# Optimization experiments

Hardware: AMD Instinct MI355X
Metric: run time of the kernel (lower is better)

The kernel has to match this reference:

```python
import jax, jax.numpy as jnp
import numpy as np

N, E = 50000, 800000
IN_F, HID, OUT, HEADS = 128, 64, 128, 4
NEG_SLOPE = 0.2


def setup_inputs() -> dict:
    key = jax.random.key(0)
    ks = jax.random.split(key, 10)
    s = 0.05
    return {
        "x": jax.random.normal(ks[0], (N, IN_F), dtype=jnp.float32),
        "edge_index": jax.random.randint(ks[1], (2, E), 0, N, dtype=jnp.int64),
        "W1": jax.random.normal(ks[2], (IN_F, HEADS * HID), dtype=jnp.float32) * s,
        "att_src1": jax.random.normal(ks[3], (HEADS, HID), dtype=jnp.float32) * s,
        "att_dst1": jax.random.normal(ks[4], (HEADS, HID), dtype=jnp.float32) * s,
        "b1": jnp.zeros((HEADS * HID,), dtype=jnp.float32),
        "W2": jax.random.normal(ks[5], (HEADS * HID, OUT), dtype=jnp.float32) * s,
        "att_src2": jax.random.normal(ks[6], (1, OUT), dtype=jnp.float32) * s,
        "att_dst2": jax.random.normal(ks[7], (1, OUT), dtype=jnp.float32) * s,
        "b2": jnp.zeros((OUT,), dtype=jnp.float32),
    }


def _gat_layer(x, W, a_src, a_dst, b, src, dst, heads, out_c):
    n = x.shape[0]
    h = (x @ W).reshape(n, heads, out_c)              # [N, H, C]
    alpha_s = jnp.einsum("nhc,hc->nh", h, a_src)       # [N, H]
    alpha_d = jnp.einsum("nhc,hc->nh", h, a_dst)
    e = jax.nn.leaky_relu(alpha_s[src] + alpha_d[dst], NEG_SLOPE)  # [E, H]
    # scatter-softmax over edges grouped by destination node
    m = jax.ops.segment_max(e, dst, num_segments=n)
    ex = jnp.exp(e - m[dst])
    denom = jax.ops.segment_sum(ex, dst, num_segments=n)
    alpha = ex / denom[dst]                            # [E, H]
    out = jax.ops.segment_sum(alpha[:, :, None] * h[src], dst, num_segments=n)
    return out.reshape(n, heads * out_c) + b


def reference(x, edge_index, W1, att_src1, att_dst1, b1, W2, att_src2, att_dst2, b2):
    n = x.shape[0]
    loop = jnp.arange(n, dtype=edge_index.dtype)       # PyG add_self_loops=True
    src = jnp.concatenate([edge_index[0], loop])
    dst = jnp.concatenate([edge_index[1], loop])
    h = _gat_layer(x, W1, att_src1, att_dst1, b1, src, dst, HEADS, HID)
    h = jax.nn.elu(h)
    out = _gat_layer(h, W2, att_src2, att_dst2, b2, src, dst, 1, OUT)
    return out
```

## Files before the change

kernel.cpp:

```cpp
#include <hip/hip_runtime.h>
#include <hip/hip_bf16.h>

#define NEG_SLOPE 0.2f

typedef short bf16x8 __attribute__((ext_vector_type(8)));
typedef float f32x4 __attribute__((ext_vector_type(4)));
typedef float f32x2 __attribute__((ext_vector_type(2)));

__device__ __forceinline__ float bf2f(unsigned short u) {
    return __uint_as_float(((unsigned int)u) << 16);
}
__device__ __forceinline__ unsigned short f2bf(float f) {
    unsigned int x = __float_as_uint(f);
    unsigned int lsb = (x >> 16) & 1u;
    x += 0x7fffu + lsb;
    return (unsigned short)(x >> 16);
}
__device__ __forceinline__ f32x2 upk(unsigned int u) {
    f32x2 r;
    r.x = __uint_as_float(u << 16);
    r.y = __uint_as_float(u & 0xffff0000u);
    return r;
}

__global__ void cast_w_kernel(const float* __restrict__ W, unsigned short* __restrict__ Wt,
                              int K, int NC) {
    int idx = blockIdx.x * 256 + threadIdx.x;
    if (idx >= K * NC) return;
    int k = idx / NC, n = idx % NC;
    Wt[(size_t)n * K + k] = f2bf(W[idx]);
}


__global__ void degree_kernel(const int* __restrict__ ei, int E, int N,
                              int* __restrict__ deg) {
    int e = blockIdx.x * blockDim.x + threadIdx.x;
    int EA = E + N;
    if (e >= EA) return;
    int dst = (e < E) ? ei[E + e] : (e - E);
    atomicAdd(&deg[dst], 1);
}

__global__ void scan_local(const int* __restrict__ deg, int* __restrict__ offs,
                           int* __restrict__ bsum, int N) {
    __shared__ int wsum[16];
    int tid = threadIdx.x;
    int lane = tid & 63;
    int wave = tid >> 6;
    int i = blockIdx.x * 1024 + tid;
    int v = (i < N) ? deg[i] : 0;
    int x = v;
    #pragma unroll
    for (int off = 1; off < 64; off <<= 1) {
        int t = __shfl_up(x, off);
        if (lane >= off) x += t;
    }
    if (lane == 63) wsum[wave] = x;
    __syncthreads();
    if (wave == 0 && lane < 16) {
        int w = wsum[lane];
        #pragma unroll
        for (int off = 1; off < 16; off <<= 1) {
            int t = __shfl_up(w, off);
            if (lane >= off) w += t;
        }
        wsum[lane] = w;
    }
    __syncthreads();
    int wexcl = (wave > 0) ? wsum[wave - 1] : 0;
    if (i <= N) offs[i] = wexcl + x - v;
    if (tid == 0) bsum[blockIdx.x] = wsum[15];
}

__global__ void scan_bsums(int* __restrict__ bsum, int nb) {
    __shared__ int wsum[16];
    int tid = threadIdx.x;
    int lane = tid & 63;
    int wave = tid >> 6;
    int v = (tid < nb) ? bsum[tid] : 0;
    int x = v;
    #pragma unroll
    for (int off = 1; off < 64; off <<= 1) {
        int t = __shfl_up(x, off);
        if (lane >= off) x += t;
    }
    if (lane == 63) wsum[wave] = x;
    __syncthreads();
    if (wave == 0 && lane < 16) {
        int w = wsum[lane];
        #pragma unroll
        for (int off = 1; off < 16; off <<= 1) {
            int t = __shfl_up(w, off);
            if (lane >= off) w += t;
        }
        wsum[lane] = w;
    }
    __syncthreads();
    int wexcl = (wave > 0) ? wsum[wave - 1] : 0;
    if (tid < nb) bsum[tid] = wexcl + x - v;
}

__global__ void scan_add(int* __restrict__ offs, const int* __restrict__ bsum, int N) {
    int i = blockIdx.x * 1024 + threadIdx.x;
    if (i <= N) offs[i] += bsum[blockIdx.x];
}

__global__ void scatter_kernel(const int* __restrict__ ei, int E, int N,
                               const int* __restrict__ offs, int* __restrict__ cnt,
                               int* __restrict__ col) {
    int e = blockIdx.x * blockDim.x + threadIdx.x;
    int EA = E + N;
    if (e >= EA) return;
    int s, d;
    if (e < E) { s = ei[e]; d = ei[E + e]; }
    else       { s = d = e - E; }
    int pos = offs[d] + atomicAdd(&cnt[d], 1);
    col[pos] = s;
}

__global__ void gemm1_mfma(const float* __restrict__ A,
                           const unsigned short* __restrict__ Wt,
                           const float* __restrict__ att_s, const float* __restrict__ att_d,
                           unsigned short* __restrict__ hb,
                           float* __restrict__ as, float* __restrict__ ad, int M) {
    int wave = threadIdx.x >> 6;
    int lane = threadIdx.x & 63;
    int quad = lane >> 4;
    int l16 = lane & 15;
    int m0 = blockIdx.x * 64 + wave * 16;
    int rowc = min(m0 + l16, M - 1);
    bf16x8 a[4];
    const float* ap = A + (size_t)rowc * 128 + quad * 8;
    #pragma unroll
    for (int kc = 0; kc < 4; ++kc) {
        float4 f0 = *(const float4*)(ap + kc * 32);
        float4 f1 = *(const float4*)(ap + kc * 32 + 4);
        bf16x8 v;
        v[0] = (short)f2bf(f0.x); v[1] = (short)f2bf(f0.y);
        v[2] = (short)f2bf(f0.z); v[3] = (short)f2bf(f0.w);
        v[4] = (short)f2bf(f1.x); v[5] = (short)f2bf(f1.y);
        v[6] = (short)f2bf(f1.z); v[7] = (short)f2bf(f1.w);
        a[kc] = v;
    }
    f32x4 acc[16];
    #pragma unroll
    for (int nt = 0; nt < 16; ++nt) {
        f32x4 c = {0.f, 0.f, 0.f, 0.f};
        const unsigned short* bp = Wt + (size_t)(nt * 16 + l16) * 128 + quad * 8;
        #pragma unroll
        for (int kc = 0; kc < 4; ++kc) {
            bf16x8 b = *(const bf16x8*)(bp + kc * 32);
            c = __builtin_amdgcn_mfma_f32_16x16x32_bf16(a[kc], b, c, 0, 0, 0);
        }
        acc[nt] = c;
    }
    float asv[16], adv[16];
    #pragma unroll
    for (int nt = 0; nt < 16; ++nt) {
        asv[nt] = att_s[nt * 16 + l16];
        adv[nt] = att_d[nt * 16 + l16];
    }
    int srow0 = m0 + quad * 4;
    #pragma unroll
    for (int r = 0; r < 4; ++r) {
        int srow = srow0 + r;
        bool ok = srow < M;
        if (ok) {
            #pragma unroll
            for (int nt = 0; nt < 16; ++nt)
                hb[(size_t)srow * 256 + nt * 16 + l16] = f2bf(acc[nt][r]);
        }
        #pragma unroll
        for (int h = 0; h < 4; ++h) {
            float ps = acc[4 * h][r] * asv[4 * h] + acc[4 * h + 1][r] * asv[4 * h + 1]
                     + acc[4 * h + 2][r] * asv[4 * h + 2] + acc[4 * h + 3][r] * asv[4 * h + 3];
            float pd = acc[4 * h][r] * adv[4 * h] + acc[4 * h + 1][r] * adv[4 * h + 1]
                     + acc[4 * h + 2][r] * adv[4 * h + 2] + acc[4 * h + 3][r] * adv[4 * h + 3];
            #pragma unroll
            for (int off = 1; off < 16; off <<= 1) {
                ps += __shfl_xor(ps, off);
                pd += __shfl_xor(pd, off);
            }
            if (ok && l16 == 0) {
                as[srow * 4 + h] = ps;
                ad[srow * 4 + h] = pd;
            }
        }
    }
}

__global__ void gemm2_mfma(const unsigned short* __restrict__ Ab,
                           const unsigned short* __restrict__ Wt,
                           const float* __restrict__ att_s, const float* __restrict__ att_d,
                           unsigned short* __restrict__ hb,
                           float* __restrict__ as, float* __restrict__ ad, int M) {
    int wave = threadIdx.x >> 6;
    int lane = threadIdx.x & 63;
    int quad = lane >> 4;
    int l16 = lane & 15;
    int m0 = blockIdx.x * 64 + wave * 16;
    int rowc = min(m0 + l16, M - 1);
    bf16x8 a[8];
    const unsigned short* ap = Ab + (size_t)rowc * 256 + quad * 8;
    #pragma unroll
    for (int kc = 0; kc < 8; ++kc) a[kc] = *(const bf16x8*)(ap + kc * 32);
    f32x4 acc[8];
    #pragma unroll
    for (int nt = 0; nt < 8; ++nt) {
        f32x4 c = {0.f, 0.f, 0.f, 0.f};
        const unsigned short* bp = Wt + (size_t)(nt * 16 + l16) * 256 + quad * 8;
        #pragma unroll
        for (int kc = 0; kc < 8; ++kc) {
            bf16x8 b = *(const bf16x8*)(bp + kc * 32);
            c = __builtin_amdgcn_mfma_f32_16x16x32_bf16(a[kc], b, c, 0, 0, 0);
        }
        acc[nt] = c;
    }
    float asv[8], adv[8];
    #pragma unroll
    for (int nt = 0; nt < 8; ++nt) {
        asv[nt] = att_s[nt * 16 + l16];
        adv[nt] = att_d[nt * 16 + l16];
    }
    int srow0 = m0 + quad * 4;
    #pragma unroll
    for (int r = 0; r < 4; ++r) {
        int srow = srow0 + r;
        bool ok = srow < M;
        if (ok) {
            #pragma unroll
            for (int nt = 0; nt < 8; ++nt)
                hb[(size_t)srow * 128 + nt * 16 + l16] = f2bf(acc[nt][r]);
        }
        float ps = 0.f, pd = 0.f;
        #pragma unroll
        for (int nt = 0; nt < 8; ++nt) {
            ps = fmaf(acc[nt][r], asv[nt], ps);
            pd = fmaf(acc[nt][r], adv[nt], pd);
        }
        #pragma unroll
        for (int off = 1; off < 16; off <<= 1) {
            ps += __shfl_xor(ps, off);
            pd += __shfl_xor(pd, off);
        }
        if (ok && l16 == 0) { as[srow] = ps; ad[srow] = pd; }
    }
}

__global__ void agg1_kernel(const unsigned short* __restrict__ hb,
                            const float* __restrict__ as,
                            const float* __restrict__ ad,
                            const int* __restrict__ offs, const int* __restrict__ col,
                            const float* __restrict__ b1,
                            unsigned short* __restrict__ out, int N) {
    int node = blockIdx.x * 4 + (threadIdx.x >> 6);
    if (node >= N) return;
    int lane = threadIdx.x & 63;
    int half = lane >> 5;
    int sub  = lane & 31;
    int head = sub >> 3;
    int c0 = sub * 8;
    float adv = ad[node * 4 + head];
    int beg = offs[node], end = offs[node + 1];
    float d = 0.f;
    f32x2 acc[4] = {};
    int j = beg + half;
    for (; j + 6 < end; j += 8) {
        int s0 = col[j];
        int s1 = col[j + 2];
        int s2 = col[j + 4];
        int s3 = col[j + 6];
        uint4 g0 = *(const uint4*)(hb + (size_t)s0 * 256 + c0);
        uint4 g1 = *(const uint4*)(hb + (size_t)s1 * 256 + c0);
        uint4 g2 = *(const uint4*)(hb + (size_t)s2 * 256 + c0);
        uint4 g3 = *(const uint4*)(hb + (size_t)s3 * 256 + c0);
        float e0 = as[s0 * 4 + head] + adv;
        float e1 = as[s1 * 4 + head] + adv;
        float e2 = as[s2 * 4 + head] + adv;
        float e3 = as[s3 * 4 + head] + adv;
        e0 = (e0 > 0.f) ? e0 : NEG_SLOPE * e0;
        e1 = (e1 > 0.f) ? e1 : NEG_SLOPE * e1;
        e2 = (e2 > 0.f) ? e2 : NEG_SLOPE * e2;
        e3 = (e3 > 0.f) ? e3 : NEG_SLOPE * e3;
        float p0 = __expf(e0), p1 = __expf(e1), p2 = __expf(e2), p3 = __expf(e3);
        d += (p0 + p1) + (p2 + p3);
        const unsigned int* w0 = (const unsigned int*)&g0;
        const unsigned int* w1 = (const unsigned int*)&g1;
        const unsigned int* w2 = (const unsigned int*)&g2;
        const unsigned int* w3 = (const unsigned int*)&g3;
        f32x2 v0 = {p0, p0}, v1 = {p1, p1}, v2 = {p2, p2}, v3 = {p3, p3};
        #pragma unroll
        for (int i = 0; i < 4; ++i) {
            acc[i] = __builtin_elementwise_fma(v0, upk(w0[i]), acc[i]);
            acc[i] = __builtin_elementwise_fma(v1, upk(w1[i]), acc[i]);
            acc[i] = __builtin_elementwise_fma(v2, upk(w2[i]), acc[i]);
            acc[i] = __builtin_elementwise_fma(v3, upk(w3[i]), acc[i]);
        }
    }
    for (; j + 2 < end; j += 4) {
        int s0 = col[j];
        int s1 = col[j + 2];
        uint4 g0 = *(const uint4*)(hb + (size_t)s0 * 256 + c0);
        uint4 g1 = *(const uint4*)(hb + (size_t)s1 * 256 + c0);
        float e0 = as[s0 * 4 + head] + adv;
        float e1 = as[s1 * 4 + head] + adv;
        e0 = (e0 > 0.f) ? e0 : NEG_SLOPE * e0;
        e1 = (e1 > 0.f) ? e1 : NEG_SLOPE * e1;
        float p0 = __expf(e0), p1 = __expf(e1);
        d += p0 + p1;
        const unsigned int* w0 = (const unsigned int*)&g0;
        const unsigned int* w1 = (const unsigned int*)&g1;
        f32x2 v0 = {p0, p0}, v1 = {p1, p1};
        #pragma unroll
        for (int i = 0; i < 4; ++i) {
            acc[i] = __builtin_elementwise_fma(v0, upk(w0[i]), acc[i]);
            acc[i] = __builtin_elementwise_fma(v1, upk(w1[i]), acc[i]);
        }
    }
    for (; j < end; j += 2) {
        int s = col[j];
        uint4 g = *(const uint4*)(hb + (size_t)s * 256 + c0);
        float e = as[s * 4 + head] + adv;
        e = (e > 0.f) ? e : NEG_SLOPE * e;
        float p = __expf(e);
        d += p;
        const unsigned int* w = (const unsigned int*)&g;
        f32x2 v = {p, p};
        #pragma unroll
        for (int i = 0; i < 4; ++i)
            acc[i] = __builtin_elementwise_fma(v, upk(w[i]), acc[i]);
    }
    d += __shfl_xor(d, 32);
    #pragma unroll
    for (int i = 0; i < 4; ++i) {
        acc[i].x += __shfl_xor(acc[i].x, 32);
        acc[i].y += __shfl_xor(acc[i].y, 32);
    }
    if (half == 0) {
        float inv = 1.f / d;
        float4 bb0 = *(const float4*)(b1 + c0);
        float4 bb1 = *(const float4*)(b1 + c0 + 4);
        float av[8] = {acc[0].x, acc[0].y, acc[1].x, acc[1].y,
                       acc[2].x, acc[2].y, acc[3].x, acc[3].y};
        float bb[8] = {bb0.x, bb0.y, bb0.z, bb0.w, bb1.x, bb1.y, bb1.z, bb1.w};
        unsigned short o[8];
        #pragma unroll
        for (int i = 0; i < 8; ++i) {
            float v = av[i] * inv + bb[i];
            v = (v > 0.f) ? v : (__expf(v) - 1.f);
            o[i] = f2bf(v);
        }
        ushort4 p0 = {o[0], o[1], o[2], o[3]};
        ushort4 p1 = {o[4], o[5], o[6], o[7]};
        *(ushort4*)(out + (size_t)node * 256 + c0) = p0;
        *(ushort4*)(out + (size_t)node * 256 + c0 + 4) = p1;
    }
}

__global__ void agg2_kernel(const unsigned short* __restrict__ hb,
                            const float* __restrict__ as,
                            const float* __restrict__ ad,
                            const int* __restrict__ offs, const int* __restrict__ col,
                            const float* __restrict__ b2,
                            float* __restrict__ out, int N) {
    int node = blockIdx.x * 4 + (threadIdx.x >> 6);
    if (node >= N) return;
    int lane = threadIdx.x & 63;
    int q   = lane >> 4;
    int sub = lane & 15;
    int c0 = sub * 8;
    float adv = ad[node];
    int beg = offs[node], end = offs[node + 1];
    float d = 0.f;
    f32x2 acc[4] = {};
    int j = beg + q;
    for (; j + 4 < end; j += 8) {
        int s0 = col[j];
        int s1 = col[j + 4];
        uint4 g0 = *(const uint4*)(hb + (size_t)s0 * 128 + c0);
        uint4 g1 = *(const uint4*)(hb + (size_t)s1 * 128 + c0);
        float e0 = as[s0] + adv;
        float e1 = as[s1] + adv;
        e0 = (e0 > 0.f) ? e0 : NEG_SLOPE * e0;
        e1 = (e1 > 0.f) ? e1 : NEG_SLOPE * e1;
        float p0 = __expf(e0), p1 = __expf(e1);
        d += p0 + p1;
        const unsigned int* w0 = (const unsigned int*)&g0;
        const unsigned int* w1 = (const unsigned int*)&g1;
        f32x2 v0 = {p0, p0}, v1 = {p1, p1};
        #pragma unroll
        for (int i = 0; i < 4; ++i) {
            acc[i] = __builtin_elementwise_fma(v0, upk(w0[i]), acc[i]);
            acc[i] = __builtin_elementwise_fma(v1, upk(w1[i]), acc[i]);
        }
    }
    for (; j < end; j += 4) {
        int s = col[j];
        uint4 g = *(const uint4*)(hb + (size_t)s * 128 + c0);
        float e = as[s] + adv;
        e = (e > 0.f) ? e : NEG_SLOPE * e;
        float p = __expf(e);
        d += p;
        const unsigned int* w = (const unsigned int*)&g;
        f32x2 v = {p, p};
        #pragma unroll
        for (int i = 0; i < 4; ++i)
            acc[i] = __builtin_elementwise_fma(v, upk(w[i]), acc[i]);
    }
    d += __shfl_xor(d, 16);
    d += __shfl_xor(d, 32);
    #pragma unroll
    for (int i = 0; i < 4; ++i) {
        acc[i].x += __shfl_xor(acc[i].x, 16);
        acc[i].x += __shfl_xor(acc[i].x, 32);
        acc[i].y += __shfl_xor(acc[i].y, 16);
        acc[i].y += __shfl_xor(acc[i].y, 32);
    }
    if (lane < 16) {
        float inv = 1.f / d;
        float4 bb0 = *(const float4*)(b2 + c0);
        float4 bb1 = *(const float4*)(b2 + c0 + 4);
        float av[8] = {acc[0].x, acc[0].y, acc[1].x, acc[1].y,
                       acc[2].x, acc[2].y, acc[3].x, acc[3].y};
        float bb[8] = {bb0.x, bb0.y, bb0.z, bb0.w, bb1.x, bb1.y, bb1.z, bb1.w};
        float o[8];
        #pragma unroll
        for (int i = 0; i < 8; ++i) o[i] = av[i] * inv + bb[i];
        *(float4*)(out + (size_t)node * 128 + c0) = make_float4(o[0], o[1], o[2], o[3]);
        *(float4*)(out + (size_t)node * 128 + c0 + 4) = make_float4(o[4], o[5], o[6], o[7]);
    }
}


extern "C" void kernel_launch(void* const* d_in, const int* in_sizes, int n_in,
                              void* d_out, int out_size, void* d_ws, size_t ws_size,
                              hipStream_t stream) {
    const float* x    = (const float*)d_in[0];
    const int*   ei   = (const int*)d_in[1];
    const float* W1   = (const float*)d_in[2];
    const float* at_s1 = (const float*)d_in[3];
    const float* at_d1 = (const float*)d_in[4];
    const float* b1   = (const float*)d_in[5];
    const float* W2   = (const float*)d_in[6];
    const float* at_s2 = (const float*)d_in[7];
    const float* at_d2 = (const float*)d_in[8];
    const float* b2   = (const float*)d_in[9];
    float* out = (float*)d_out;

    const int N  = in_sizes[0] / 128;
    const int E  = in_sizes[1] / 2;
    const int EA = E + N;

    char* ws = (char*)d_ws;
    size_t off = 0;
    auto alloc = [&](size_t bytes) -> void* {
        void* p = ws + off;
        off += (bytes + 255) & ~(size_t)255;
        return p;
    };
    unsigned short* wt1  = (unsigned short*)alloc((size_t)256 * 128 * 2);
    unsigned short* wt2  = (unsigned short*)alloc((size_t)128 * 256 * 2);
    unsigned short* h1b  = (unsigned short*)alloc((size_t)N * 256 * 2);
    unsigned short* h1ab = (unsigned short*)alloc((size_t)N * 256 * 2);
    unsigned short* h2b  = (unsigned short*)alloc((size_t)N * 128 * 2);
    float* as1 = (float*)alloc((size_t)N * 4 * 4);
    float* ad1 = (float*)alloc((size_t)N * 4 * 4);
    float* as2 = (float*)alloc((size_t)N * 4);
    float* ad2 = (float*)alloc((size_t)N * 4);
    int* deg  = (int*)alloc((size_t)2 * N * 4);
    int* cnt  = deg + N;
    int* offs = (int*)alloc((size_t)(N + 1) * 4);
    int* bsum = (int*)alloc((size_t)1024 * 4);
    int* col  = (int*)alloc((size_t)EA * 4);

    const int nb = (N + 1 + 1023) / 1024;

    hipMemsetAsync(deg, 0, (size_t)2 * N * 4, stream);
    cast_w_kernel<<<(128 * 256 + 255) / 256, 256, 0, stream>>>(W1, wt1, 128, 256);
    cast_w_kernel<<<(256 * 128 + 255) / 256, 256, 0, stream>>>(W2, wt2, 256, 128);
    degree_kernel<<<(EA + 255) / 256, 256, 0, stream>>>(ei, E, N, deg);
    scan_local<<<nb, 1024, 0, stream>>>(deg, offs, bsum, N);
    scan_bsums<<<1, 1024, 0, stream>>>(bsum, nb);
    scan_add<<<nb, 1024, 0, stream>>>(offs, bsum, N);
    scatter_kernel<<<(EA + 255) / 256, 256, 0, stream>>>(ei, E, N, offs, cnt, col);

    gemm1_mfma<<<(N + 63) / 64, 256, 0, stream>>>(x, wt1, at_s1, at_d1, h1b, as1, ad1, N);
    agg1_kernel<<<(N + 3) / 4, 256, 0, stream>>>(h1b, as1, ad1, offs, col, b1, h1ab, N);

    gemm2_mfma<<<(N + 63) / 64, 256, 0, stream>>>(h1ab, wt2, at_s2, at_d2, h2b, as2, ad2, N);
    agg2_kernel<<<(N + 3) / 4, 256, 0, stream>>>(h2b, as2, ad2, offs, col, b2, out, N);
}
```

Before: 351.6 us.

## Slice GEMM outputs into 32-column panels and aggregate one panel per pass

The GEMM epilogues now write the projected features in a sliced layout, with 32-column panels stored contiguously per node. The aggregation kernels run one grid pass per panel (8 for layer 1, 4 for layer 2), so each pass gathers a smaller, more cache-resident slice. Each wave now spreads edges across 16 lanes groups, with 4 lanes per 64-byte row. The aim is better L2 hit rates on the random source gathers. The cost is recomputing the attention weights and reading the edge lists once per pass. Separately, the two weight-cast kernels are merged and the block-sum scan is folded into scan_add, which cuts two launches.

```diff
diff --git a/kernel.cpp b/kernel.cpp
--- a/kernel.cpp
+++ b/kernel.cpp
@@ -7,9 +7,6 @@
 typedef float f32x4 __attribute__((ext_vector_type(4)));
 typedef float f32x2 __attribute__((ext_vector_type(2)));
 
-__device__ __forceinline__ float bf2f(unsigned short u) {
-    return __uint_as_float(((unsigned int)u) << 16);
-}
 __device__ __forceinline__ unsigned short f2bf(float f) {
     unsigned int x = __float_as_uint(f);
     unsigned int lsb = (x >> 16) & 1u;
@@ -23,12 +20,17 @@
     return r;
 }
 
-__global__ void cast_w_kernel(const float* __restrict__ W, unsigned short* __restrict__ Wt,
-                              int K, int NC) {
+__global__ void cast_w_both(const float* __restrict__ W1, const float* __restrict__ W2,
+                            unsigned short* __restrict__ wt1, unsigned short* __restrict__ wt2) {
     int idx = blockIdx.x * 256 + threadIdx.x;
-    if (idx >= K * NC) return;
-    int k = idx / NC, n = idx % NC;
-    Wt[(size_t)n * K + k] = f2bf(W[idx]);
+    if (idx < 128 * 256) {
+        int k = idx >> 8, n = idx & 255;
+        wt1[(size_t)n * 128 + k] = f2bf(W1[idx]);
+    } else {
+        int j = idx - 128 * 256;
+        int k = j >> 7, n = j & 127;
+        wt2[(size_t)n * 256 + k] = f2bf(W2[j]);
+    }
 }
 
 
@@ -72,37 +74,19 @@
     if (tid == 0) bsum[blockIdx.x] = wsum[15];
 }
 
-__global__ void scan_bsums(int* __restrict__ bsum, int nb) {
-    __shared__ int wsum[16];
-    int tid = threadIdx.x;
-    int lane = tid & 63;
-    int wave = tid >> 6;
-    int v = (tid < nb) ? bsum[tid] : 0;
+__global__ void scan_add(int* __restrict__ offs, const int* __restrict__ bsum,
+                         int N, int nb) {
+    int lane = threadIdx.x & 63;
+    int v = (lane < nb) ? bsum[lane] : 0;
     int x = v;
     #pragma unroll
     for (int off = 1; off < 64; off <<= 1) {
         int t = __shfl_up(x, off);
         if (lane >= off) x += t;
     }
-    if (lane == 63) wsum[wave] = x;
-    __syncthreads();
-    if (wave == 0 && lane < 16) {
-        int w = wsum[lane];
-        #pragma unroll
-        for (int off = 1; off < 16; off <<= 1) {
-            int t = __shfl_up(w, off);
-            if (lane >= off) w += t;
-        }
-        wsum[lane] = w;
-    }
-    __syncthreads();
-    int wexcl = (wave > 0) ? wsum[wave - 1] : 0;
-    if (tid < nb) bsum[tid] = wexcl + x - v;
-}
-
-__global__ void scan_add(int* __restrict__ offs, const int* __restrict__ bsum, int N) {
+    int excl = __shfl(x - v, blockIdx.x);
     int i = blockIdx.x * 1024 + threadIdx.x;
-    if (i <= N) offs[i] += bsum[blockIdx.x];
+    if (i <= N) offs[i] += excl;
 }
 
 __global__ void scatter_kernel(const int* __restrict__ ei, int E, int N,
@@ -121,7 +105,7 @@
 __global__ void gemm1_mfma(const float* __restrict__ A,
                            const unsigned short* __restrict__ Wt,
                            const float* __restrict__ att_s, const float* __restrict__ att_d,
-                           unsigned short* __restrict__ hb,
+                           unsigned short* __restrict__ hs,
                            float* __restrict__ as, float* __restrict__ ad, int M) {
     int wave = threadIdx.x >> 6;
     int lane = threadIdx.x & 63;
@@ -168,7 +152,8 @@
         if (ok) {
             #pragma unroll
             for (int nt = 0; nt < 16; ++nt)
-                hb[(size_t)srow * 256 + nt * 16 + l16] = f2bf(acc[nt][r]);
+                hs[((size_t)(nt >> 1) * M + srow) * 32 + (nt & 1) * 16 + l16] =
+                    f2bf(acc[nt][r]);
         }
         #pragma unroll
         for (int h = 0; h < 4; ++h) {
@@ -192,7 +177,7 @@
 __global__ void gemm2_mfma(const unsigned short* __restrict__ Ab,
                            const unsigned short* __restrict__ Wt,
                            const float* __restrict__ att_s, const float* __restrict__ att_d,
-                           unsigned short* __restrict__ hb,
+                           unsigned short* __restrict__ hs,
                            float* __restrict__ as, float* __restrict__ ad, int M) {
     int wave = threadIdx.x >> 6;
     int lane = threadIdx.x & 63;
@@ -230,7 +215,8 @@
         if (ok) {
             #pragma unroll
             for (int nt = 0; nt < 8; ++nt)
-                hb[(size_t)srow * 128 + nt * 16 + l16] = f2bf(acc[nt][r]);
+                hs[((size_t)(nt >> 1) * M + srow) * 32 + (nt & 1) * 16 + l16] =
+                    f2bf(acc[nt][r]);
         }
         float ps = 0.f, pd = 0.f;
         #pragma unroll
@@ -247,61 +233,32 @@
     }
 }
 
-__global__ void agg1_kernel(const unsigned short* __restrict__ hb,
+__global__ void agg1_kernel(const unsigned short* __restrict__ hs,
                             const float* __restrict__ as,
                             const float* __restrict__ ad,
                             const int* __restrict__ offs, const int* __restrict__ col,
                             const float* __restrict__ b1,
-                            unsigned short* __restrict__ out, int N) {
-    int node = blockIdx.x * 4 + (threadIdx.x >> 6);
+                            unsigned short* __restrict__ out, int N, int NB) {
+    int pass = blockIdx.x / NB;
+    int nb = blockIdx.x - pass * NB;
+    int wave = threadIdx.x >> 6;
+    int node = nb * 4 + wave;
     if (node >= N) return;
     int lane = threadIdx.x & 63;
-    int half = lane >> 5;
-    int sub  = lane & 31;
-    int head = sub >> 3;
-    int c0 = sub * 8;
+    int sub = lane >> 2;
+    int cl = lane & 3;
+    int head = pass >> 1;
     float adv = ad[node * 4 + head];
     int beg = offs[node], end = offs[node + 1];
+    const unsigned short* hp = hs + (size_t)pass * N * 32 + cl * 8;
     float d = 0.f;
     f32x2 acc[4] = {};
-    int j = beg + half;
-    for (; j + 6 < end; j += 8) {
+    int j = beg + sub;
+    for (; j + 16 < end; j += 32) {
         int s0 = col[j];
-        int s1 = col[j + 2];
-        int s2 = col[j + 4];
-        int s3 = col[j + 6];
-        uint4 g0 = *(const uint4*)(hb + (size_t)s0 * 256 + c0);
-        uint4 g1 = *(const uint4*)(hb + (size_t)s1 * 256 + c0);
-        uint4 g2 = *(const uint4*)(hb + (size_t)s2 * 256 + c0);
-        uint4 g3 = *(const uint4*)(hb + (size_t)s3 * 256 + c0);
-        float e0 = as[s0 * 4 + head] + adv;
-        float e1 = as[s1 * 4 + head] + adv;
-        float e2 = as[s2 * 4 + head] + adv;
-        float e3 = as[s3 * 4 + head] + adv;
-        e0 = (e0 > 0.f) ? e0 : NEG_SLOPE * e0;
-        e1 = (e1 > 0.f) ? e1 : NEG_SLOPE * e1;
-        e2 = (e2 > 0.f) ? e2 : NEG_SLOPE * e2;
-        e3 = (e3 > 0.f) ? e3 : NEG_SLOPE * e3;
-        float p0 = __expf(e0), p1 = __expf(e1), p2 = __expf(e2), p3 = __expf(e3);
-        d += (p0 + p1) + (p2 + p3);
-        const unsigned int* w0 = (const unsigned int*)&g0;
-        const unsigned int* w1 = (const unsigned int*)&g1;
-        const unsigned int* w2 = (const unsigned int*)&g2;
-        const unsigned int* w3 = (const unsigned int*)&g3;
-        f32x2 v0 = {p0, p0}, v1 = {p1, p1}, v2 = {p2, p2}, v3 = {p3, p3};
-        #pragma unroll
-        for (int i = 0; i < 4; ++i) {
-            acc[i] = __builtin_elementwise_fma(v0, upk(w0[i]), acc[i]);
-            acc[i] = __builtin_elementwise_fma(v1, upk(w1[i]), acc[i]);
-            acc[i] = __builtin_elementwise_fma(v2, upk(w2[i]), acc[i]);
-            acc[i] = __builtin_elementwise_fma(v3, upk(w3[i]), acc[i]);
-        }
-    }
-    for (; j + 2 < end; j += 4) {
-        int s0 = col[j];
-        int s1 = col[j + 2];
-        uint4 g0 = *(const uint4*)(hb + (size_t)s0 * 256 + c0);
-        uint4 g1 = *(const uint4*)(hb + (size_t)s1 * 256 + c0);
+        int s1 = col[j + 16];
+        uint4 g0 = *(const uint4*)(hp + (size_t)s0 * 32);
+        uint4 g1 = *(const uint4*)(hp + (size_t)s1 * 32);
         float e0 = as[s0 * 4 + head] + adv;
         float e1 = as[s1 * 4 + head] + adv;
         e0 = (e0 > 0.f) ? e0 : NEG_SLOPE * e0;
@@ -317,9 +274,9 @@
             acc[i] = __builtin_elementwise_fma(v1, upk(w1[i]), acc[i]);
         }
     }
-    for (; j < end; j += 2) {
+    for (; j < end; j += 16) {
         int s = col[j];
-        uint4 g = *(const uint4*)(hb + (size_t)s * 256 + c0);
+        uint4 g = *(const uint4*)(hp + (size_t)s * 32);
         float e = as[s * 4 + head] + adv;
         e = (e > 0.f) ? e : NEG_SLOPE * e;
         float p = __expf(e);
@@ -330,14 +287,18 @@
         for (int i = 0; i < 4; ++i)
             acc[i] = __builtin_elementwise_fma(v, upk(w[i]), acc[i]);
     }
-    d += __shfl_xor(d, 32);
-    #pragma unroll
-    for (int i = 0; i < 4; ++i) {
-        acc[i].x += __shfl_xor(acc[i].x, 32);
-        acc[i].y += __shfl_xor(acc[i].y, 32);
-    }
-    if (half == 0) {
+    #pragma unroll
+    for (int off = 4; off < 64; off <<= 1) {
+        d += __shfl_xor(d, off);
+        #pragma unroll
+        for (int i = 0; i < 4; ++i) {
+            acc[i].x += __shfl_xor(acc[i].x, off);
+            acc[i].y += __shfl_xor(acc[i].y, off);
+        }
+    }
+    if (sub == 0) {
         float inv = 1.f / d;
+        int c0 = pass * 32 + cl * 8;
         float4 bb0 = *(const float4*)(b1 + c0);
         float4 bb1 = *(const float4*)(b1 + c0 + 4);
         float av[8] = {acc[0].x, acc[0].y, acc[1].x, acc[1].y,
@@ -357,28 +318,31 @@
     }
 }
 
-__global__ void agg2_kernel(const unsigned short* __restrict__ hb,
+__global__ void agg2_kernel(const unsigned short* __restrict__ hs,
                             const float* __restrict__ as,
                             const float* __restrict__ ad,
                             const int* __restrict__ offs, const int* __restrict__ col,
                             const float* __restrict__ b2,
-                            float* __restrict__ out, int N) {
-    int node = blockIdx.x * 4 + (threadIdx.x >> 6);
+                            float* __restrict__ out, int N, int NB) {
+    int pass = blockIdx.x / NB;
+    int nb = blockIdx.x - pass * NB;
+    int wave = threadIdx.x >> 6;
+    int node = nb * 4 + wave;
     if (node >= N) return;
     int lane = threadIdx.x & 63;
-    int q   = lane >> 4;
-    int sub = lane & 15;
-    int c0 = sub * 8;
+    int sub = lane >> 2;
+    int cl = lane & 3;
     float adv = ad[node];
     int beg = offs[node], end = offs[node + 1];
+    const unsigned short* hp = hs + (size_t)pass * N * 32 + cl * 8;
     float d = 0.f;
     f32x2 acc[4] = {};
-    int j = beg + q;
-    for (; j + 4 < end; j += 8) {
+    int j = beg + sub;
+    for (; j + 16 < end; j += 32) {
         int s0 = col[j];
-        int s1 = col[j + 4];
-        uint4 g0 = *(const uint4*)(hb + (size_t)s0 * 128 + c0);
-        uint4 g1 = *(const uint4*)(hb + (size_t)s1 * 128 + c0);
+        int s1 = col[j + 16];
+        uint4 g0 = *(const uint4*)(hp + (size_t)s0 * 32);
+        uint4 g1 = *(const uint4*)(hp + (size_t)s1 * 32);
         float e0 = as[s0] + adv;
         float e1 = as[s1] + adv;
         e0 = (e0 > 0.f) ? e0 : NEG_SLOPE * e0;
@@ -394,9 +358,9 @@
             acc[i] = __builtin_elementwise_fma(v1, upk(w1[i]), acc[i]);
         }
     }
-    for (; j < end; j += 4) {
+    for (; j < end; j += 16) {
         int s = col[j];
-        uint4 g = *(const uint4*)(hb + (size_t)s * 128 + c0);
+        uint4 g = *(const uint4*)(hp + (size_t)s * 32);
         float e = as[s] + adv;
         e = (e > 0.f) ? e : NEG_SLOPE * e;
         float p = __expf(e);
@@ -407,27 +371,29 @@
         for (int i = 0; i < 4; ++i)
             acc[i] = __builtin_elementwise_fma(v, upk(w[i]), acc[i]);
     }
-    d += __shfl_xor(d, 16);
-    d += __shfl_xor(d, 32);
-    #pragma unroll
-    for (int i = 0; i < 4; ++i) {
-        acc[i].x += __shfl_xor(acc[i].x, 16);
-        acc[i].x += __shfl_xor(acc[i].x, 32);
-        acc[i].y += __shfl_xor(acc[i].y, 16);
-        acc[i].y += __shfl_xor(acc[i].y, 32);
-    }
-    if (lane < 16) {
+    #pragma unroll
+    for (int off = 4; off < 64; off <<= 1) {
+        d += __shfl_xor(d, off);
+        #pragma unroll
+        for (int i = 0; i < 4; ++i) {
+            acc[i].x += __shfl_xor(acc[i].x, off);
+            acc[i].y += __shfl_xor(acc[i].y, off);
+        }
+    }
+    if (sub == 0) {
         float inv = 1.f / d;
+        int c0 = pass * 32 + cl * 8;
         float4 bb0 = *(const float4*)(b2 + c0);
         float4 bb1 = *(const float4*)(b2 + c0 + 4);
         float av[8] = {acc[0].x, acc[0].y, acc[1].x, acc[1].y,
                        acc[2].x, acc[2].y, acc[3].x, acc[3].y};
         float bb[8] = {bb0.x, bb0.y, bb0.z, bb0.w, bb1.x, bb1.y, bb1.z, bb1.w};
-        float o[8];
-        #pragma unroll
-        for (int i = 0; i < 8; ++i) o[i] = av[i] * inv + bb[i];
-        *(float4*)(out + (size_t)node * 128 + c0) = make_float4(o[0], o[1], o[2], o[3]);
-        *(float4*)(out + (size_t)node * 128 + c0 + 4) = make_float4(o[4], o[5], o[6], o[7]);
+        *(float4*)(out + (size_t)node * 128 + c0) =
+            make_float4(av[0] * inv + bb[0], av[1] * inv + bb[1],
+                        av[2] * inv + bb[2], av[3] * inv + bb[3]);
+        *(float4*)(out + (size_t)node * 128 + c0 + 4) =
+            make_float4(av[4] * inv + bb[4], av[5] * inv + bb[5],
+                        av[6] * inv + bb[6], av[7] * inv + bb[7]);
     }
 }
 
@@ -460,9 +426,9 @@
     };
     unsigned short* wt1  = (unsigned short*)alloc((size_t)256 * 128 * 2);
     unsigned short* wt2  = (unsigned short*)alloc((size_t)128 * 256 * 2);
-    unsigned short* h1b  = (unsigned short*)alloc((size_t)N * 256 * 2);
+    unsigned short* h1s  = (unsigned short*)alloc((size_t)N * 256 * 2);
     unsigned short* h1ab = (unsigned short*)alloc((size_t)N * 256 * 2);
-    unsigned short* h2b  = (unsigned short*)alloc((size_t)N * 128 * 2);
+    unsigned short* h2s  = (unsigned short*)alloc((size_t)N * 128 * 2);
     float* as1 = (float*)alloc((size_t)N * 4 * 4);
     float* ad1 = (float*)alloc((size_t)N * 4 * 4);
     float* as2 = (float*)alloc((size_t)N * 4);
@@ -474,19 +440,18 @@
     int* col  = (int*)alloc((size_t)EA * 4);
 
     const int nb = (N + 1 + 1023) / 1024;
+    const int NB = (N + 3) / 4;
 
     hipMemsetAsync(deg, 0, (size_t)2 * N * 4, stream);
-    cast_w_kernel<<<(128 * 256 + 255) / 256, 256, 0, stream>>>(W1, wt1, 128, 256);
-    cast_w_kernel<<<(256 * 128 + 255) / 256, 256, 0, stream>>>(W2, wt2, 256, 128);
+    cast_w_both<<<(2 * 128 * 256 + 255) / 256, 256, 0, stream>>>(W1, W2, wt1, wt2);
     degree_kernel<<<(EA + 255) / 256, 256, 0, stream>>>(ei, E, N, deg);
     scan_local<<<nb, 1024, 0, stream>>>(deg, offs, bsum, N);
-    scan_bsums<<<1, 1024, 0, stream>>>(bsum, nb);
-    scan_add<<<nb, 1024, 0, stream>>>(offs, bsum, N);
+    scan_add<<<nb, 1024, 0, stream>>>(offs, bsum, N, nb);
     scatter_kernel<<<(EA + 255) / 256, 256, 0, stream>>>(ei, E, N, offs, cnt, col);
 
-    gemm1_mfma<<<(N + 63) / 64, 256, 0, stream>>>(x, wt1, at_s1, at_d1, h1b, as1, ad1, N);
-    agg1_kernel<<<(N + 3) / 4, 256, 0, stream>>>(h1b, as1, ad1, offs, col, b1, h1ab, N);
-
-    gemm2_mfma<<<(N + 63) / 64, 256, 0, stream>>>(h1ab, wt2, at_s2, at_d2, h2b, as2, ad2, N);
-    agg2_kernel<<<(N + 3) / 4, 256, 0, stream>>>(h2b, as2, ad2, offs, col, b2, out, N);
-}
+    gemm1_mfma<<<(N + 63) / 64, 256, 0, stream>>>(x, wt1, at_s1, at_d1, h1s, as1, ad1, N);
+    agg1_kernel<<<8 * NB, 256, 0, stream>>>(h1s, as1, ad1, offs, col, b1, h1ab, N, NB);
+
+    gemm2_mfma<<<(N + 63) / 64, 256, 0, stream>>>(h1ab, wt2, at_s2, at_d2, h2s, as2, ad2, N);
+    agg2_kernel<<<4 * NB, 256, 0, stream>>>(h2s, as2, ad2, offs, col, b2, out, N, NB);
+}
```

Result: slower. 499.4 us (+42.0%).

## Precompute layer-1 edge exponentials in scatter, drop atomics and scan kernel

Applied to the files above, without the earlier changes.

The degree pass now records each edge's slot index, so the scatter needs no second atomic and the counter array goes away. The scatter runs after gemm1 and computes the four per-head unnormalised attention exponentials per edge, packed as fp16 into a CSR-ordered array. agg1 then reads those values with coalesced loads instead of gathering as1 randomly and doing exp per lane. The block-sum scan is merged into scan_add, the two weight casts become one launch, and col stores pre-shifted byte offsets. In exchange it adds an extra 8 bytes per edge of write and read traffic and fp16 rounding of the exponentials, which could overflow if the logits are large.

```diff
diff --git a/kernel.cpp b/kernel.cpp
--- a/kernel.cpp
+++ b/kernel.cpp
@@ -7,9 +7,6 @@
 typedef float f32x4 __attribute__((ext_vector_type(4)));
 typedef float f32x2 __attribute__((ext_vector_type(2)));
 
-__device__ __forceinline__ float bf2f(unsigned short u) {
-    return __uint_as_float(((unsigned int)u) << 16);
-}
 __device__ __forceinline__ unsigned short f2bf(float f) {
     unsigned int x = __float_as_uint(f);
     unsigned int lsb = (x >> 16) & 1u;
@@ -22,23 +19,35 @@
     r.y = __uint_as_float(u & 0xffff0000u);
     return r;
 }
-
-__global__ void cast_w_kernel(const float* __restrict__ W, unsigned short* __restrict__ Wt,
-                              int K, int NC) {
+__device__ __forceinline__ unsigned short f2h(float f) {
+    _Float16 h = (_Float16)f;
+    return *(unsigned short*)&h;
+}
+__device__ __forceinline__ float h2f(unsigned short u) {
+    _Float16 h = *(_Float16*)&u;
+    return (float)h;
+}
+
+__global__ void cast_w_both(const float* __restrict__ W1, const float* __restrict__ W2,
+                            unsigned short* __restrict__ wt1, unsigned short* __restrict__ wt2) {
     int idx = blockIdx.x * 256 + threadIdx.x;
-    if (idx >= K * NC) return;
-    int k = idx / NC, n = idx % NC;
-    Wt[(size_t)n * K + k] = f2bf(W[idx]);
-}
-
+    if (idx < 128 * 256) {
+        int k = idx >> 8, n = idx & 255;
+        wt1[(size_t)n * 128 + k] = f2bf(W1[idx]);
+    } else {
+        int j = idx - 128 * 256;
+        int k = j >> 7, n = j & 127;
+        wt2[(size_t)n * 256 + k] = f2bf(W2[j]);
+    }
+}
 
 __global__ void degree_kernel(const int* __restrict__ ei, int E, int N,
-                              int* __restrict__ deg) {
+                              int* __restrict__ deg, int* __restrict__ idx) {
     int e = blockIdx.x * blockDim.x + threadIdx.x;
     int EA = E + N;
     if (e >= EA) return;
     int dst = (e < E) ? ei[E + e] : (e - E);
-    atomicAdd(&deg[dst], 1);
+    idx[e] = atomicAdd(&deg[dst], 1);
 }
 
 __global__ void scan_local(const int* __restrict__ deg, int* __restrict__ offs,
@@ -72,50 +81,44 @@
     if (tid == 0) bsum[blockIdx.x] = wsum[15];
 }
 
-__global__ void scan_bsums(int* __restrict__ bsum, int nb) {
-    __shared__ int wsum[16];
-    int tid = threadIdx.x;
-    int lane = tid & 63;
-    int wave = tid >> 6;
-    int v = (tid < nb) ? bsum[tid] : 0;
+__global__ void scan_add(int* __restrict__ offs, const int* __restrict__ bsum,
+                         int N, int nb) {
+    int lane = threadIdx.x & 63;
+    int v = (lane < nb) ? bsum[lane] : 0;
     int x = v;
     #pragma unroll
     for (int off = 1; off < 64; off <<= 1) {
         int t = __shfl_up(x, off);
         if (lane >= off) x += t;
     }
-    if (lane == 63) wsum[wave] = x;
-    __syncthreads();
-    if (wave == 0 && lane < 16) {
-        int w = wsum[lane];
-        #pragma unroll
-        for (int off = 1; off < 16; off <<= 1) {
-            int t = __shfl_up(w, off);
-            if (lane >= off) w += t;
-        }
-        wsum[lane] = w;
-    }
-    __syncthreads();
-    int wexcl = (wave > 0) ? wsum[wave - 1] : 0;
-    if (tid < nb) bsum[tid] = wexcl + x - v;
-}
-
-__global__ void scan_add(int* __restrict__ offs, const int* __restrict__ bsum, int N) {
+    int excl = __shfl(x - v, blockIdx.x);
     int i = blockIdx.x * 1024 + threadIdx.x;
-    if (i <= N) offs[i] += bsum[blockIdx.x];
+    if (i <= N) offs[i] += excl;
 }
 
 __global__ void scatter_kernel(const int* __restrict__ ei, int E, int N,
-                               const int* __restrict__ offs, int* __restrict__ cnt,
-                               int* __restrict__ col) {
+                               const int* __restrict__ offs, const int* __restrict__ idx,
+                               const float* __restrict__ as1, const float* __restrict__ ad1,
+                               int* __restrict__ colb, uint2* __restrict__ p1) {
     int e = blockIdx.x * blockDim.x + threadIdx.x;
     int EA = E + N;
     if (e >= EA) return;
     int s, d;
     if (e < E) { s = ei[e]; d = ei[E + e]; }
     else       { s = d = e - E; }
-    int pos = offs[d] + atomicAdd(&cnt[d], 1);
-    col[pos] = s;
+    int pos = offs[d] + idx[e];
+    colb[pos] = s << 9;
+    float4 av = *(const float4*)(as1 + s * 4);
+    float4 dv = *(const float4*)(ad1 + d * 4);
+    float e0 = av.x + dv.x, e1 = av.y + dv.y, e2 = av.z + dv.z, e3 = av.w + dv.w;
+    e0 = (e0 > 0.f) ? e0 : NEG_SLOPE * e0;
+    e1 = (e1 > 0.f) ? e1 : NEG_SLOPE * e1;
+    e2 = (e2 > 0.f) ? e2 : NEG_SLOPE * e2;
+    e3 = (e3 > 0.f) ? e3 : NEG_SLOPE * e3;
+    uint2 q;
+    q.x = (unsigned int)f2h(__expf(e0)) | ((unsigned int)f2h(__expf(e1)) << 16);
+    q.y = (unsigned int)f2h(__expf(e2)) | ((unsigned int)f2h(__expf(e3)) << 16);
+    p1[pos] = q;
 }
 
 __global__ void gemm1_mfma(const float* __restrict__ A,
@@ -248,9 +251,8 @@
 }
 
 __global__ void agg1_kernel(const unsigned short* __restrict__ hb,
-                            const float* __restrict__ as,
-                            const float* __restrict__ ad,
-                            const int* __restrict__ offs, const int* __restrict__ col,
+                            const int* __restrict__ colb, const uint2* __restrict__ p1,
+                            const int* __restrict__ offs,
                             const float* __restrict__ b1,
                             unsigned short* __restrict__ out, int N) {
     int node = blockIdx.x * 4 + (threadIdx.x >> 6);
@@ -259,36 +261,39 @@
     int half = lane >> 5;
     int sub  = lane & 31;
     int head = sub >> 3;
-    int c0 = sub * 8;
-    float adv = ad[node * 4 + head];
+    int c0b = sub * 16;
+    const char* hpc = (const char*)hb;
     int beg = offs[node], end = offs[node + 1];
     float d = 0.f;
     f32x2 acc[4] = {};
     int j = beg + half;
     for (; j + 6 < end; j += 8) {
-        int s0 = col[j];
-        int s1 = col[j + 2];
-        int s2 = col[j + 4];
-        int s3 = col[j + 6];
-        uint4 g0 = *(const uint4*)(hb + (size_t)s0 * 256 + c0);
-        uint4 g1 = *(const uint4*)(hb + (size_t)s1 * 256 + c0);
-        uint4 g2 = *(const uint4*)(hb + (size_t)s2 * 256 + c0);
-        uint4 g3 = *(const uint4*)(hb + (size_t)s3 * 256 + c0);
-        float e0 = as[s0 * 4 + head] + adv;
-        float e1 = as[s1 * 4 + head] + adv;
-        float e2 = as[s2 * 4 + head] + adv;
-        float e3 = as[s3 * 4 + head] + adv;
-        e0 = (e0 > 0.f) ? e0 : NEG_SLOPE * e0;
-        e1 = (e1 > 0.f) ? e1 : NEG_SLOPE * e1;
-        e2 = (e2 > 0.f) ? e2 : NEG_SLOPE * e2;
-        e3 = (e3 > 0.f) ? e3 : NEG_SLOPE * e3;
-        float p0 = __expf(e0), p1 = __expf(e1), p2 = __expf(e2), p3 = __expf(e3);
-        d += (p0 + p1) + (p2 + p3);
+        int o0 = colb[j] + c0b;
+        int o1 = colb[j + 2] + c0b;
+        int o2 = colb[j + 4] + c0b;
+        int o3 = colb[j + 6] + c0b;
+        uint2 q0 = p1[j];
+        uint2 q1 = p1[j + 2];
+        uint2 q2 = p1[j + 4];
+        uint2 q3 = p1[j + 6];
+        uint4 g0 = *(const uint4*)(hpc + o0);
+        uint4 g1 = *(const uint4*)(hpc + o1);
+        uint4 g2 = *(const uint4*)(hpc + o2);
+        uint4 g3 = *(const uint4*)(hpc + o3);
+        unsigned int u0 = (head & 2) ? q0.y : q0.x;
+        unsigned int u1 = (head & 2) ? q1.y : q1.x;
+        unsigned int u2 = (head & 2) ? q2.y : q2.x;
+        unsigned int u3 = (head & 2) ? q3.y : q3.x;
+        float p0 = h2f((unsigned short)((head & 1) ? (u0 >> 16) : (u0 & 0xffff)));
+        float p1v = h2f((unsigned short)((head & 1) ? (u1 >> 16) : (u1 & 0xffff)));
+        float p2 = h2f((unsigned short)((head & 1) ? (u2 >> 16) : (u2 & 0xffff)));
+        float p3 = h2f((unsigned short)((head & 1) ? (u3 >> 16) : (u3 & 0xffff)));
+        d += (p0 + p1v) + (p2 + p3);
         const unsigned int* w0 = (const unsigned int*)&g0;
         const unsigned int* w1 = (const unsigned int*)&g1;
         const unsigned int* w2 = (const unsigned int*)&g2;
         const unsigned int* w3 = (const unsigned int*)&g3;
-        f32x2 v0 = {p0, p0}, v1 = {p1, p1}, v2 = {p2, p2}, v3 = {p3, p3};
+        f32x2 v0 = {p0, p0}, v1 = {p1v, p1v}, v2 = {p2, p2}, v3 = {p3, p3};
         #pragma unroll
         for (int i = 0; i < 4; ++i) {
             acc[i] = __builtin_elementwise_fma(v0, upk(w0[i]), acc[i]);
@@ -297,13 +302,72 @@
             acc[i] = __builtin_elementwise_fma(v3, upk(w3[i]), acc[i]);
         }
     }
-    for (; j + 2 < end; j += 4) {
-        int s0 = col[j];
-        int s1 = col[j + 2];
-        uint4 g0 = *(const uint4*)(hb + (size_t)s0 * 256 + c0);
-        uint4 g1 = *(const uint4*)(hb + (size_t)s1 * 256 + c0);
-        float e0 = as[s0 * 4 + head] + adv;
-        float e1 = as[s1 * 4 + head] + adv;
+    for (; j < end; j += 2) {
+        int o = colb[j] + c0b;
+        uint2 q = p1[j];
+        uint4 g = *(const uint4*)(hpc + o);
+        unsigned int u = (head & 2) ? q.y : q.x;
+        float p = h2f((unsigned short)((head & 1) ? (u >> 16) : (u & 0xffff)));
+        d += p;
+        const unsigned int* w = (const unsigned int*)&g;
+        f32x2 v = {p, p};
+        #pragma unroll
+        for (int i = 0; i < 4; ++i)
+            acc[i] = __builtin_elementwise_fma(v, upk(w[i]), acc[i]);
+    }
+    d += __shfl_xor(d, 32);
+    #pragma unroll
+    for (int i = 0; i < 4; ++i) {
+        acc[i].x += __shfl_xor(acc[i].x, 32);
+        acc[i].y += __shfl_xor(acc[i].y, 32);
+    }
+    if (half == 0) {
+        float inv = 1.f / d;
+        int c0 = sub * 8;
+        float4 bb0 = *(const float4*)(b1 + c0);
+        float4 bb1 = *(const float4*)(b1 + c0 + 4);
+        float av[8] = {acc[0].x, acc[0].y, acc[1].x, acc[1].y,
+                       acc[2].x, acc[2].y, acc[3].x, acc[3].y};
+        float bb[8] = {bb0.x, bb0.y, bb0.z, bb0.w, bb1.x, bb1.y, bb1.z, bb1.w};
+        unsigned short o[8];
+        #pragma unroll
+        for (int i = 0; i < 8; ++i) {
+            float v = av[i] * inv + bb[i];
+            v = (v > 0.f) ? v : (__expf(v) - 1.f);
+            o[i] = f2bf(v);
+        }
+        ushort4 q0 = {o[0], o[1], o[2], o[3]};
+        ushort4 q1 = {o[4], o[5], o[6], o[7]};
+        *(ushort4*)(out + (size_t)node * 256 + c0) = q0;
+        *(ushort4*)(out + (size_t)node * 256 + c0 + 4) = q1;
+    }
+}
+
+__global__ void agg2_kernel(const unsigned short* __restrict__ hb,
+                            const float* __restrict__ as,
+                            const float* __restrict__ ad,
+                            const int* __restrict__ offs, const int* __restrict__ colb,
+                            const float* __restrict__ b2,
+                            float* __restrict__ out, int N) {
+    int node = blockIdx.x * 4 + (threadIdx.x >> 6);
+    if (node >= N) return;
+    int lane = threadIdx.x & 63;
+    int q   = lane >> 4;
+    int sub = lane & 15;
+    int c0b = sub * 16;
+    const char* hpc = (const char*)hb;
+    float adv = ad[node];
+    int beg = offs[node], end = offs[node + 1];
+    float d = 0.f;
+    f32x2 acc[4] = {};
+    int j = beg + q;
+    for (; j + 4 < end; j += 8) {
+        int cb0 = colb[j];
+        int cb1 = colb[j + 4];
+        uint4 g0 = *(const uint4*)(hpc + (cb0 >> 1) + c0b);
+        uint4 g1 = *(const uint4*)(hpc + (cb1 >> 1) + c0b);
+        float e0 = as[cb0 >> 9] + adv;
+        float e1 = as[cb1 >> 9] + adv;
         e0 = (e0 > 0.f) ? e0 : NEG_SLOPE * e0;
         e1 = (e1 > 0.f) ? e1 : NEG_SLOPE * e1;
         float p0 = __expf(e0), p1 = __expf(e1);
@@ -317,10 +381,10 @@
             acc[i] = __builtin_elementwise_fma(v1, upk(w1[i]), acc[i]);
         }
     }
-    for (; j < end; j += 2) {
-        int s = col[j];
-        uint4 g = *(const uint4*)(hb + (size_t)s * 256 + c0);
-        float e = as[s * 4 + head] + adv;
+    for (; j < end; j += 4) {
+        int cb = colb[j];
+        uint4 g = *(const uint4*)(hpc + (cb >> 1) + c0b);
+        float e = as[cb >> 9] + adv;
         e = (e > 0.f) ? e : NEG_SLOPE * e;
         float p = __expf(e);
         d += p;
@@ -330,83 +394,6 @@
         for (int i = 0; i < 4; ++i)
             acc[i] = __builtin_elementwise_fma(v, upk(w[i]), acc[i]);
     }
-    d += __shfl_xor(d, 32);
-    #pragma unroll
-    for (int i = 0; i < 4; ++i) {
-        acc[i].x += __shfl_xor(acc[i].x, 32);
-        acc[i].y += __shfl_xor(acc[i].y, 32);
-    }
-    if (half == 0) {
-        float inv = 1.f / d;
-        float4 bb0 = *(const float4*)(b1 + c0);
-        float4 bb1 = *(const float4*)(b1 + c0 + 4);
-        float av[8] = {acc[0].x, acc[0].y, acc[1].x, acc[1].y,
-                       acc[2].x, acc[2].y, acc[3].x, acc[3].y};
-        float bb[8] = {bb0.x, bb0.y, bb0.z, bb0.w, bb1.x, bb1.y, bb1.z, bb1.w};
-        unsigned short o[8];
-        #pragma unroll
-        for (int i = 0; i < 8; ++i) {
-            float v = av[i] * inv + bb[i];
-            v = (v > 0.f) ? v : (__expf(v) - 1.f);
-            o[i] = f2bf(v);
-        }
-        ushort4 p0 = {o[0], o[1], o[2], o[3]};
-        ushort4 p1 = {o[4], o[5], o[6], o[7]};
-        *(ushort4*)(out + (size_t)node * 256 + c0) = p0;
-        *(ushort4*)(out + (size_t)node * 256 + c0 + 4) = p1;
-    }
-}
-
-__global__ void agg2_kernel(const unsigned short* __restrict__ hb,
-                            const float* __restrict__ as,
-                            const float* __restrict__ ad,
-                            const int* __restrict__ offs, const int* __restrict__ col,
-                            const float* __restrict__ b2,
-                            float* __restrict__ out, int N) {
-    int node = blockIdx.x * 4 + (threadIdx.x >> 6);
-    if (node >= N) return;
-    int lane = threadIdx.x & 63;
-    int q   = lane >> 4;
-    int sub = lane & 15;
-    int c0 = sub * 8;
-    float adv = ad[node];
-    int beg = offs[node], end = offs[node + 1];
-    float d = 0.f;
-    f32x2 acc[4] = {};
-    int j = beg + q;
-    for (; j + 4 < end; j += 8) {
-        int s0 = col[j];
-        int s1 = col[j + 4];
-        uint4 g0 = *(const uint4*)(hb + (size_t)s0 * 128 + c0);
-        uint4 g1 = *(const uint4*)(hb + (size_t)s1 * 128 + c0);
-        float e0 = as[s0] + adv;
-        float e1 = as[s1] + adv;
-        e0 = (e0 > 0.f) ? e0 : NEG_SLOPE * e0;
-        e1 = (e1 > 0.f) ? e1 : NEG_SLOPE * e1;
-        float p0 = __expf(e0), p1 = __expf(e1);
-        d += p0 + p1;
-        const unsigned int* w0 = (const unsigned int*)&g0;
-        const unsigned int* w1 = (const unsigned int*)&g1;
-        f32x2 v0 = {p0, p0}, v1 = {p1, p1};
-        #pragma unroll
-        for (int i = 0; i < 4; ++i) {
-            acc[i] = __builtin_elementwise_fma(v0, upk(w0[i]), acc[i]);
-            acc[i] = __builtin_elementwise_fma(v1, upk(w1[i]), acc[i]);
-        }
-    }
-    for (; j < end; j += 4) {
-        int s = col[j];
-        uint4 g = *(const uint4*)(hb + (size_t)s * 128 + c0);
-        float e = as[s] + adv;
-        e = (e > 0.f) ? e : NEG_SLOPE * e;
-        float p = __expf(e);
-        d += p;
-        const unsigned int* w = (const unsigned int*)&g;
-        f32x2 v = {p, p};
-        #pragma unroll
-        for (int i = 0; i < 4; ++i)
-            acc[i] = __builtin_elementwise_fma(v, upk(w[i]), acc[i]);
-    }
     d += __shfl_xor(d, 16);
     d += __shfl_xor(d, 32);
     #pragma unroll
@@ -418,16 +405,18 @@
     }
     if (lane < 16) {
         float inv = 1.f / d;
+        int c0 = sub * 8;
         float4 bb0 = *(const float4*)(b2 + c0);
         float4 bb1 = *(const float4*)(b2 + c0 + 4);
         float av[8] = {acc[0].x, acc[0].y, acc[1].x, acc[1].y,
                        acc[2].x, acc[2].y, acc[3].x, acc[3].y};
         float bb[8] = {bb0.x, bb0.y, bb0.z, bb0.w, bb1.x, bb1.y, bb1.z, bb1.w};
-        float o[8];
-        #pragma unroll
-        for (int i = 0; i < 8; ++i) o[i] = av[i] * inv + bb[i];
-        *(float4*)(out + (size_t)node * 128 + c0) = make_float4(o[0], o[1], o[2], o[3]);
-        *(float4*)(out + (size_t)node * 128 + c0 + 4) = make_float4(o[4], o[5], o[6], o[7]);
+        *(float4*)(out + (size_t)node * 128 + c0) =
+            make_float4(av[0] * inv + bb[0], av[1] * inv + bb[1],
+                        av[2] * inv + bb[2], av[3] * inv + bb[3]);
+        *(float4*)(out + (size_t)node * 128 + c0 + 4) =
+            make_float4(av[4] * inv + bb[4], av[5] * inv + bb[5],
+                        av[6] * inv + bb[6], av[7] * inv + bb[7]);
     }
 }
 
@@ -467,26 +456,26 @@
     float* ad1 = (float*)alloc((size_t)N * 4 * 4);
     float* as2 = (float*)alloc((size_t)N * 4);
     float* ad2 = (float*)alloc((size_t)N * 4);
-    int* deg  = (int*)alloc((size_t)2 * N * 4);
-    int* cnt  = deg + N;
+    int* deg  = (int*)alloc((size_t)N * 4);
+    int* idx  = (int*)alloc((size_t)EA * 4);
     int* offs = (int*)alloc((size_t)(N + 1) * 4);
     int* bsum = (int*)alloc((size_t)1024 * 4);
-    int* col  = (int*)alloc((size_t)EA * 4);
+    int* colb = (int*)alloc((size_t)EA * 4);
+    uint2* p1 = (uint2*)alloc((size_t)EA * 8);
 
     const int nb = (N + 1 + 1023) / 1024;
 
-    hipMemsetAsync(deg, 0, (size_t)2 * N * 4, stream);
-    cast_w_kernel<<<(128 * 256 + 255) / 256, 256, 0, stream>>>(W1, wt1, 128, 256);
-    cast_w_kernel<<<(256 * 128 + 255) / 256, 256, 0, stream>>>(W2, wt2, 256, 128);
-    degree_kernel<<<(EA + 255) / 256, 256, 0, stream>>>(ei, E, N, deg);
+    hipMemsetAsync(deg, 0, (size_t)N * 4, stream);
+    cast_w_both<<<(2 * 128 * 256 + 255) / 256, 256, 0, stream>>>(W1, W2, wt1, wt2);
+    degree_kernel<<<(EA + 255) / 256, 256, 0, stream>>>(ei, E, N, deg, idx);
     scan_local<<<nb, 1024, 0, stream>>>(deg, offs, bsum, N);
-    scan_bsums<<<1, 1024, 0, stream>>>(bsum, nb);
-    scan_add<<<nb, 1024, 0, stream>>>(offs, bsum, N);
-    scatter_kernel<<<(EA + 255) / 256, 256, 0, stream>>>(ei, E, N, offs, cnt, col);
+    scan_add<<<nb, 1024, 0, stream>>>(offs, bsum, N, nb);
 
     gemm1_mfma<<<(N + 63) / 64, 256, 0, stream>>>(x, wt1, at_s1, at_d1, h1b, as1, ad1, N);
-    agg1_kernel<<<(N + 3) / 4, 256, 0, stream>>>(h1b, as1, ad1, offs, col, b1, h1ab, N);
+    scatter_kernel<<<(EA + 255) / 256, 256, 0, stream>>>(ei, E, N, offs, idx, as1, ad1,
+                                                         colb, p1);
+    agg1_kernel<<<(N + 3) / 4, 256, 0, stream>>>(h1b, colb, p1, offs, b1, h1ab, N);
 
     gemm2_mfma<<<(N + 63) / 64, 256, 0, stream>>>(h1ab, wt2, at_s2, at_d2, h2b, as2, ad2, N);
-    agg2_kernel<<<(N + 3) / 4, 256, 0, stream>>>(h2b, as2, ad2, offs, col, b2, out, N);
-}
+    agg2_kernel<<<(N + 3) / 4, 256, 0, stream>>>(h2b, as2, ad2, offs, colb, b2, out, N);
+}
```

Result: faster. 330.5 us (-6.0%).
